# Optimization experiments

Measured on AMD Instinct MI355X. Metric: run time of the kernel, lower is better.

Reference implementation:

```python
import jax, jax.numpy as jnp
import numpy as np

B, T, V, E = 1024, 100, 9173, 100
H1, H2 = 128, 512


def _gru(x, k, rk, b):
    # Keras GRU v2 (reset_after=True). x: [B,T,D], k: [D,3H], rk: [H,3H], b: [2,3H]
    bi, br = b[0], b[1]
    xs = jnp.swapaxes(jnp.einsum('btd,dh->bth', x, k) + bi, 0, 1)  # [T,B,3H]
    H = rk.shape[0]
    h0 = jnp.zeros((x.shape[0], H), x.dtype)

    def step(h, xt):
        inner = h @ rk + br
        xz, xr, xh = jnp.split(xt, 3, -1)
        rz, rr, rh = jnp.split(inner, 3, -1)
        z = jax.nn.sigmoid(xz + rz)
        r = jax.nn.sigmoid(xr + rr)
        hh = jnp.tanh(xh + r * rh)
        h = z * h + (1.0 - z) * hh
        return h, h

    _, ys = jax.lax.scan(step, h0, xs)
    return jnp.swapaxes(ys, 0, 1)  # [B,T,H]


def _lstm(x, k, rk, b, reverse=False):
    # Keras LSTM, gate order i,f,c,o. x: [B,T,D], k: [D,4H], rk: [H,4H], b: [4H]
    if reverse:
        x = x[:, ::-1]
    xs = jnp.swapaxes(jnp.einsum('btd,dh->bth', x, k) + b, 0, 1)  # [T,B,4H]
    H = rk.shape[0]
    Bb = x.shape[0]
    carry0 = (jnp.zeros((Bb, H), x.dtype), jnp.zeros((Bb, H), x.dtype))

    def step(carry, xt):
        h, c = carry
        g = xt + h @ rk
        i, f, cc, o = jnp.split(g, 4, -1)
        c = jax.nn.sigmoid(f) * c + jax.nn.sigmoid(i) * jnp.tanh(cc)
        h = jax.nn.sigmoid(o) * jnp.tanh(c)
        return (h, c), h

    _, ys = jax.lax.scan(step, carry0, xs)
    ys = jnp.swapaxes(ys, 0, 1)
    if reverse:
        ys = ys[:, ::-1]  # Bidirectional re-reverses backward outputs
    return ys


def setup_inputs() -> dict:
    key = jax.random.key(0)
    ks = jax.random.split(key, 32)
    s = 0.05
    p = {}
    p['text'] = jax.random.randint(ks[0], (B, T), 0, V)
    p['upvote'] = jax.random.normal(ks[1], (B, 1), jnp.float32)
    p['emb'] = s * jax.random.normal(ks[2], (V, E), jnp.float32)
    # forward GRU(128)
    p['gf_k'] = s * jax.random.normal(ks[3], (E, 3 * H1), jnp.float32)
    p['gf_rk'] = s * jax.random.normal(ks[4], (H1, 3 * H1), jnp.float32)
    p['gf_b'] = s * jax.random.normal(ks[5], (2, 3 * H1), jnp.float32)
    # backward LSTM(128)
    p['lb_k'] = s * jax.random.normal(ks[6], (E, 4 * H1), jnp.float32)
    p['lb_rk'] = s * jax.random.normal(ks[7], (H1, 4 * H1), jnp.float32)
    p['lb_b'] = s * jax.random.normal(ks[8], (4 * H1,), jnp.float32)
    # GRU(512) on concat(256)
    p['g2_k'] = s * jax.random.normal(ks[9], (2 * H1, 3 * H2), jnp.float32)
    p['g2_rk'] = s * jax.random.normal(ks[10], (H2, 3 * H2), jnp.float32)
    p['g2_b'] = s * jax.random.normal(ks[11], (2, 3 * H2), jnp.float32)
    # LSTM(512)
    p['l2_k'] = s * jax.random.normal(ks[12], (H2, 4 * H2), jnp.float32)
    p['l2_rk'] = s * jax.random.normal(ks[13], (H2, 4 * H2), jnp.float32)
    p['l2_b'] = s * jax.random.normal(ks[14], (4 * H2,), jnp.float32)
    # dense heads
    p['fc1_w'] = s * jax.random.normal(ks[15], (1, 512), jnp.float32)
    p['fc1_b'] = jnp.zeros((512,), jnp.float32)
    p['d1_w'] = s * jax.random.normal(ks[16], (1024, 64), jnp.float32)
    p['d1_b'] = jnp.zeros((64,), jnp.float32)
    p['d2_w'] = s * jax.random.normal(ks[17], (64, 512), jnp.float32)
    p['d2_b'] = jnp.zeros((512,), jnp.float32)
    p['d3_w'] = s * jax.random.normal(ks[18], (512, 128), jnp.float32)
    p['d3_b'] = jnp.zeros((128,), jnp.float32)
    p['rat_w'] = s * jax.random.normal(ks[19], (128, 5), jnp.float32)
    p['rat_b'] = jnp.zeros((5,), jnp.float32)
    p['rec_w'] = s * jax.random.normal(ks[20], (128, 1), jnp.float32)
    p['rec_b'] = jnp.zeros((1,), jnp.float32)
    return p


def reference(text, upvote, emb, gf_k, gf_rk, gf_b, lb_k, lb_rk, lb_b,
              g2_k, g2_rk, g2_b, l2_k, l2_rk, l2_b,
              fc1_w, fc1_b, d1_w, d1_b, d2_w, d2_b, d3_w, d3_b,
              rat_w, rat_b, rec_w, rec_b):
    x = emb[text]                                   # [B,T,E]
    fwd = _gru(x, gf_k, gf_rk, gf_b)                # [B,T,128]
    bwd = _lstm(x, lb_k, lb_rk, lb_b, reverse=True)  # [B,T,128]
    x1 = jnp.concatenate([fwd, bwd], -1)            # [B,T,256]
    x1 = _gru(x1, g2_k, g2_rk, g2_b)                # [B,T,512]
    x1 = _lstm(x1, l2_k, l2_rk, l2_b)               # [B,T,512]
    x1 = jnp.mean(x1, axis=1)                       # GlobalAveragePooling1D
    x2 = jax.nn.relu(upvote @ fc1_w + fc1_b)        # [B,512]
    h = jnp.concatenate([x1, x2], -1)               # [B,1024]
    h = jax.nn.relu(h @ d1_w + d1_b)
    h = jax.nn.relu(h @ d2_w + d2_b)
    h = jax.nn.relu(h @ d3_w + d3_b)
    rating = jax.nn.softmax(h @ rat_w + rat_b, axis=-1)
    recommend = jax.nn.sigmoid(h @ rec_w + rec_b)
    return rating, recommend
```

## Files before the change

### kernel.cpp

```cpp
#include <hip/hip_runtime.h>

typedef __attribute__((ext_vector_type(8))) short bf16x8;
typedef __attribute__((ext_vector_type(4))) float f32x4;

#define MFMA(a, b, c) __builtin_amdgcn_mfma_f32_16x16x32_bf16((a), (b), (c), 0, 0, 0)

__device__ inline short f2bf(float f) {
  unsigned u = __builtin_bit_cast(unsigned, f);
  u += 0x7fffu + ((u >> 16) & 1u);
  return (short)(u >> 16);
}
__device__ inline float bf2f(short s) {
  unsigned u = ((unsigned)(unsigned short)s) << 16;
  return __builtin_bit_cast(float, u);
}
__device__ inline float sigm(float x) { return 1.f / (1.f + expf(-x)); }

#define VM_DRAIN() asm volatile("s_waitcnt vmcnt(0)" ::: "memory")

__device__ __forceinline__ void sc_load16(const char* g0, const char* g1,
                                          const char* l0, const char* l1,
                                          bf16x8* rg, bf16x8* rl) {
  asm volatile(
      "global_load_dwordx4 %0, %16, off sc0 sc1\n\t"
      "global_load_dwordx4 %1, %16, off offset:1024 sc0 sc1\n\t"
      "global_load_dwordx4 %2, %16, off offset:2048 sc0 sc1\n\t"
      "global_load_dwordx4 %3, %16, off offset:3072 sc0 sc1\n\t"
      "global_load_dwordx4 %4, %17, off sc0 sc1\n\t"
      "global_load_dwordx4 %5, %17, off offset:1024 sc0 sc1\n\t"
      "global_load_dwordx4 %6, %17, off offset:2048 sc0 sc1\n\t"
      "global_load_dwordx4 %7, %17, off offset:3072 sc0 sc1\n\t"
      "global_load_dwordx4 %8, %18, off sc0 sc1\n\t"
      "global_load_dwordx4 %9, %18, off offset:1024 sc0 sc1\n\t"
      "global_load_dwordx4 %10, %18, off offset:2048 sc0 sc1\n\t"
      "global_load_dwordx4 %11, %18, off offset:3072 sc0 sc1\n\t"
      "global_load_dwordx4 %12, %19, off sc0 sc1\n\t"
      "global_load_dwordx4 %13, %19, off offset:1024 sc0 sc1\n\t"
      "global_load_dwordx4 %14, %19, off offset:2048 sc0 sc1\n\t"
      "global_load_dwordx4 %15, %19, off offset:3072 sc0 sc1\n\t"
      "s_waitcnt vmcnt(0)"
      : "=&v"(rg[0]), "=&v"(rg[1]), "=&v"(rg[2]), "=&v"(rg[3]),
        "=&v"(rg[4]), "=&v"(rg[5]), "=&v"(rg[6]), "=&v"(rg[7]),
        "=&v"(rl[0]), "=&v"(rl[1]), "=&v"(rl[2]), "=&v"(rl[3]),
        "=&v"(rl[4]), "=&v"(rl[5]), "=&v"(rl[6]), "=&v"(rl[7])
      : "v"(g0), "v"(g1), "v"(l0), "v"(l1)
      : "memory");
}

__device__ __forceinline__ void store_short_sys(short* p, short v) {
  int vi = (int)(unsigned short)v;
  asm volatile("global_store_short %0, %1, off sc0 sc1" :: "v"(p), "v"(vi) : "memory");
}

#define B_SZ 1024
#define T_SZ 100

#define O_GFK   0u
#define O_GFRK  (O_GFK  + 98304u)
#define O_LBK   (O_GFRK + 98304u)
#define O_LBRK  (O_LBK  + 131072u)
#define O_G2    (O_LBRK + 131072u)
#define O_L2    (O_G2   + 2359296u)
#define O_X     (O_L2   + 4194304u)
#define O_X1    (O_X    + 26214400u)
#define O_HG    (O_X1   + 52428800u)
#define O_HL    (O_HG   + 2097152u)
#define O_BAR   (O_HL   + 2097152u)
#define O_MS    (O_BAR  + 2097152u)

__global__ void pack_b(const float* __restrict__ s1, int K1,
                       const float* __restrict__ s2, int K1p,
                       int Kp, int N, short* __restrict__ dst) {
  int i = blockIdx.x * 256 + threadIdx.x;
  int total = N * Kp;
  if (i >= total) return;
  int v = i & 7, c = (i >> 3) & 15, r = i >> 7;
  int kb8 = Kp >> 3;
  int kb = r % kb8, nt = r / kb8;
  int k = kb * 8 + v, col = nt * 16 + c;
  float val;
  if (k < K1p) val = (k < K1) ? s1[k * N + col] : 0.f;
  else         val = s2[(k - K1p) * N + col];
  dst[i] = f2bf(val);
}

__global__ void embed_k(const int* __restrict__ text, const float* __restrict__ emb,
                        short* __restrict__ x) {
  int i = blockIdx.x * 256 + threadIdx.x;
  if (i >= B_SZ * T_SZ * 128) return;
  int col = i & 127, bt = i >> 7;
  float v = 0.f;
  if (col < 100) v = emb[text[bt] * 100 + col];
  x[i] = f2bf(v);
}

__global__ __launch_bounds__(512) void layer1_k(
    const short* __restrict__ x, const short* __restrict__ gfk,
    const short* __restrict__ gfrk, const float* __restrict__ gfb,
    const short* __restrict__ lbk, const short* __restrict__ lbrk,
    const float* __restrict__ lbb, short* __restrict__ x1) {
  __shared__ __attribute__((aligned(16))) short rkl[65536];
  __shared__ __attribute__((aligned(16))) short xst[16 * 136];
  __shared__ __attribute__((aligned(16))) short hst[16 * 136];
  const int wgid = blockIdx.x;
  const bool gru = wgid < 64;
  const int b0 = (gru ? wgid : wgid - 64) * 16;
  const int tid = threadIdx.x, lane = tid & 63, w = tid >> 6;
  const int c = lane & 15, g = lane >> 4;
  const int NS = gru ? 3 : 4;

  for (int i = tid; i < 16 * 136; i += 512) hst[i] = 0;

  const bf16x8* kp = (const bf16x8*)(gru ? gfk : lbk);
  const bf16x8* rpg = (const bf16x8*)(gru ? gfrk : lbrk);
  {
    bf16x8* rl8 = (bf16x8*)rkl;
    int n8 = gru ? 6144 : 8192;
    for (int i = tid; i < n8; i += 512) rl8[i] = rpg[i];
  }
  const bf16x8* rp = (const bf16x8*)rkl;

  bf16x8 kf[4][4];
  #pragma unroll
  for (int s = 0; s < 4; ++s)
    if (s < NS)
      #pragma unroll
      for (int ks = 0; ks < 4; ++ks)
        kf[s][ks] = kp[((s * 8 + w) * 16 + 4 * ks + g) * 16 + c];

  const int col = w * 16 + c;
  float bz = 0, br_ = 0, bxh = 0, brh = 0, bi_ = 0, bf_ = 0, bc_ = 0, bo_ = 0;
  if (gru) {
    bz  = gfb[col]       + gfb[384 + col];
    br_ = gfb[128 + col] + gfb[512 + col];
    bxh = gfb[256 + col];
    brh = gfb[640 + col];
  } else {
    bi_ = lbb[col]; bf_ = lbb[128 + col]; bc_ = lbb[256 + col]; bo_ = lbb[384 + col];
  }

  float hreg[4] = {0.f, 0.f, 0.f, 0.f};
  float cst[4]  = {0.f, 0.f, 0.f, 0.f};

  for (int tt = 0; tt < T_SZ; ++tt) {
    const int t = gru ? tt : (T_SZ - 1 - tt);
    __syncthreads();
    if (tid < 256) {
      int row = tid >> 4, ch = tid & 15;
      *(bf16x8*)&xst[row * 136 + ch * 8] =
          *(const bf16x8*)&x[((b0 + row) * T_SZ + t) * 128 + ch * 8];
    }
    __syncthreads();

    f32x4 acc[4];
    #pragma unroll
    for (int s = 0; s < 4; ++s) acc[s] = (f32x4){0.f, 0.f, 0.f, 0.f};

    bf16x8 ax[4], ah[4];
    #pragma unroll
    for (int ks = 0; ks < 4; ++ks) {
      ax[ks] = *(const bf16x8*)&xst[c * 136 + ks * 32 + g * 8];
      ah[ks] = *(const bf16x8*)&hst[c * 136 + ks * 32 + g * 8];
    }
    #pragma unroll
    for (int s = 0; s < 4; ++s) {
      if (s < NS) {
        int dst = (gru && s == 2) ? 3 : s;
        #pragma unroll
        for (int ks = 0; ks < 4; ++ks) {
          acc[s] = MFMA(ax[ks], kf[s][ks], acc[s]);
          bf16x8 bh = rp[((s * 8 + w) * 16 + 4 * ks + g) * 16 + c];
          acc[dst] = MFMA(ah[ks], bh, acc[dst]);
        }
      }
    }
    __syncthreads();

    if (gru) {
      #pragma unroll
      for (int j = 0; j < 4; ++j) {
        float z  = sigm(acc[0][j] + bz);
        float r  = sigm(acc[1][j] + br_);
        float hh = tanhf(acc[2][j] + bxh + r * (acc[3][j] + brh));
        float hn = z * hreg[j] + (1.f - z) * hh;
        hreg[j] = hn;
        short hb = f2bf(hn);
        int row = 4 * g + j;
        hst[row * 136 + col] = hb;
        x1[((b0 + row) * T_SZ + t) * 256 + col] = hb;
      }
    } else {
      #pragma unroll
      for (int j = 0; j < 4; ++j) {
        float i_ = acc[0][j] + bi_;
        float f_ = acc[1][j] + bf_;
        float cc = acc[2][j] + bc_;
        float o_ = acc[3][j] + bo_;
        float cn = sigm(f_) * cst[j] + sigm(i_) * tanhf(cc);
        cst[j] = cn;
        float hn = sigm(o_) * tanhf(cn);
        short hb = f2bf(hn);
        int row = 4 * g + j;
        hst[row * 136 + col] = hb;
        x1[((b0 + row) * T_SZ + t) * 256 + 128 + col] = hb;
      }
    }
  }
}

__device__ __forceinline__ void gbar16(unsigned* bar, int grp, int gen) {
  VM_DRAIN();
  __syncthreads();
  if (threadIdx.x == 0) {
    unsigned want = (unsigned)(gen + 1);
    unsigned* cnt = bar + grp * 32;
    unsigned* rel = cnt + 16;
    unsigned o = __hip_atomic_fetch_add(cnt, 1u, __ATOMIC_RELAXED, __HIP_MEMORY_SCOPE_AGENT);
    if (o == want * 16u - 1u) {
      __hip_atomic_store(rel, want, __ATOMIC_RELAXED, __HIP_MEMORY_SCOPE_AGENT);
    } else {
      unsigned tries = 0;
      while (__hip_atomic_load(rel, __ATOMIC_RELAXED, __HIP_MEMORY_SCOPE_AGENT) < want) {
        __builtin_amdgcn_s_sleep(2);
        if (++tries > (1u << 22)) break;
      }
    }
  }
  __syncthreads();
}

__global__ __launch_bounds__(512, 2) void persist2_k(
    const short* __restrict__ x1, const short* __restrict__ G2p, const float* __restrict__ g2b,
    const short* __restrict__ L2p, const float* __restrict__ l2b,
    short* __restrict__ hg, short* __restrict__ hl,
    float* __restrict__ msum, unsigned* __restrict__ bar) {
  __shared__ __attribute__((aligned(16))) short Asm[65536];
  float* XA  = (float*)Asm;
  float* XB  = (float*)&Asm[32768];

  const int wgid = blockIdx.x;
  const int rowwg = wgid >> 4, colwg = wgid & 15;
  const int b0 = rowwg * 64;
  const int tid = threadIdx.x, w = tid >> 6, lane = tid & 63;
  const int c = lane & 15, g = lane >> 4;
  const int c7 = c & 7;
  const int ehc = lane & 31;
  const int er0 = w * 8 + (lane >> 5) * 4;
  const int hcg = colwg * 32 + ehc;

  const float bz  = g2b[hcg] + g2b[1536 + hcg];
  const float br_ = g2b[512 + hcg] + g2b[2048 + hcg];
  const float bxh = g2b[1024 + hcg];
  const float brh = g2b[2560 + hcg];
  const float bi_ = l2b[hcg], bf_ = l2b[512 + hcg];
  const float bc_ = l2b[1024 + hcg], bo_ = l2b[1536 + hcg];

  const bf16x8* Gv  = (const bf16x8*)G2p;
  const bf16x8* L2v = (const bf16x8*)L2p;
  const int gw = w >> 1, ghf = w & 1;
  const int gntg = gw * 32 + colwg * 2 + ghf;
  const int lgate = w & 3, lkh = w >> 2;

  float creg[4] = {0.f, 0.f, 0.f, 0.f};
  float mreg[4] = {0.f, 0.f, 0.f, 0.f};

  for (int k = 0; k <= 100; ++k) {
    const short* hg_rd = hg + (size_t)((k + 1) & 1) * 524288;
    const short* hl_rd = hl + (size_t)(k & 1) * 524288;

    if (k < 100) {
      const bf16x8* x1v = (const bf16x8*)x1;
      #pragma unroll
      for (int it = 0; it < 4; ++it) {
        int idx = it * 512 + tid;
        int row = idx >> 5, cx = idx & 31;
        *(bf16x8*)&Asm[32768 + row * 256 + ((cx ^ (row & 7)) << 3)] =
            x1v[((size_t)(b0 + row) * T_SZ + k) * 32 + cx];
      }
    }

    bf16x8 rg[8], rl[8];
    {
      const char* bg = (const char*)hg_rd + (size_t)(b0 + w * 8) * 1024 + lane * 16;
      const char* bl = (const char*)hl_rd + (size_t)(b0 + w * 8) * 1024 + lane * 16;
      sc_load16(bg, bg + 4096, bl, bl + 4096, rg, rl);
    }
    #pragma unroll
    for (int q = 0; q < 8; ++q)
      *(bf16x8*)&Asm[(w * 8 + q) * 512 + ((lane ^ q) << 3)] = rg[q];
    __syncthreads();

    if (k < 100) {
      f32x4 acc[4], acch[4];
      if (w < 6) {
        #pragma unroll
        for (int m = 0; m < 4; ++m) {
          acc[m] = (f32x4){0.f, 0.f, 0.f, 0.f};
          acch[m] = (f32x4){0.f, 0.f, 0.f, 0.f};
        }
        #pragma unroll 6
        for (int ks = 0; ks < 24; ++ks) {
          bf16x8 b = Gv[((size_t)gntg * 96 + 4 * ks + g) * 16 + c];
          bf16x8 a[4];
          #pragma unroll
          for (int m = 0; m < 4; ++m) {
            int row = m * 16 + c;
            a[m] = (ks < 8)
                ? *(const bf16x8*)&Asm[32768 + row * 256 + (((ks * 4 + g) ^ c7) << 3)]
                : *(const bf16x8*)&Asm[row * 512 + ((((ks - 8) * 4 + g) ^ c7) << 3)];
          }
          if (w >= 4 && ks >= 8) {
            #pragma unroll
            for (int m = 0; m < 4; ++m) acch[m] = MFMA(a[m], b, acch[m]);
          } else {
            #pragma unroll
            for (int m = 0; m < 4; ++m) acc[m] = MFMA(a[m], b, acc[m]);
          }
        }
      }
      __syncthreads();

      if (w < 6) {
        #pragma unroll
        for (int m = 0; m < 4; ++m)
          #pragma unroll
          for (int j = 0; j < 4; ++j) {
            int row = m * 16 + 4 * g + j;
            if (gw < 2) XB[(gw * 64 + row) * 36 + ghf * 16 + c] = acc[m][j];
            else {
              XB[(128 + row) * 36 + ghf * 16 + c] = acc[m][j];
              XB[(192 + row) * 36 + ghf * 16 + c] = acch[m][j];
            }
          }
      }
      __syncthreads();

      short* hgw = hg + (size_t)(k & 1) * 524288;
      #pragma unroll
      for (int j = 0; j < 4; ++j) {
        int r = er0 + j;
        int xi = r * 36 + ehc;
        float z  = sigm(XB[xi] + bz);
        float rr = sigm(XB[xi + 2304] + br_);
        float hh = tanhf(XB[xi + 4608] + bxh + rr * (XB[xi + 6912] + brh));
        float hold = bf2f(Asm[r * 512 + (((hcg >> 3) ^ (r & 7)) << 3) + (hcg & 7)]);
        float hn = z * hold + (1.f - z) * hh;
        store_short_sys(&hgw[(size_t)(b0 + r) * 512 + hcg], f2bf(hn));
      }
      __syncthreads();
    }

    if (k >= 1) {
      #pragma unroll
      for (int q = 0; q < 8; ++q)
        *(bf16x8*)&Asm[32768 + (w * 8 + q) * 512 + ((lane ^ q) << 3)] = rl[q];
      __syncthreads();

      f32x4 acc[4][2];
      #pragma unroll
      for (int m = 0; m < 4; ++m)
        #pragma unroll
        for (int n = 0; n < 2; ++n) acc[m][n] = (f32x4){0.f, 0.f, 0.f, 0.f};

      const int abase = lkh ? 32768 : 0;
      #pragma unroll
      for (int ks = 0; ks < 16; ++ks) {
        bf16x8 a[4];
        #pragma unroll
        for (int m = 0; m < 4; ++m) {
          int row = m * 16 + c;
          a[m] = *(const bf16x8*)&Asm[abase + row * 512 + (((ks * 4 + g) ^ c7) << 3)];
        }
        #pragma unroll
        for (int m = 0; m < 4; ++m)
          #pragma unroll
          for (int n = 0; n < 2; ++n) {
            bf16x8 b = L2v[((size_t)(lgate * 32 + colwg * 2 + n) * 128 +
                            4 * (lkh * 16 + ks) + g) * 16 + c];
            acc[m][n] = MFMA(a[m], b, acc[m][n]);
          }
      }
      __syncthreads();

      float* Xp = lkh ? XB : XA;
      #pragma unroll
      for (int m = 0; m < 4; ++m)
        #pragma unroll
        for (int n = 0; n < 2; ++n)
          #pragma unroll
          for (int j = 0; j < 4; ++j)
            Xp[(lgate * 64 + m * 16 + 4 * g + j) * 36 + n * 16 + c] = acc[m][n][j];
      __syncthreads();

      short* hlw = hl + (size_t)((k + 1) & 1) * 524288;
      #pragma unroll
      for (int j = 0; j < 4; ++j) {
        int r = er0 + j;
        int xi = r * 36 + ehc;
        float i_ = XA[xi]        + XB[xi]        + bi_;
        float f_ = XA[xi + 2304] + XB[xi + 2304] + bf_;
        float cc = XA[xi + 4608] + XB[xi + 4608] + bc_;
        float o_ = XA[xi + 6912] + XB[xi + 6912] + bo_;
        float cn = sigm(f_) * creg[j] + sigm(i_) * tanhf(cc);
        creg[j] = cn;
        float hn = sigm(o_) * tanhf(cn);
        mreg[j] += hn;
        store_short_sys(&hlw[(size_t)(b0 + r) * 512 + hcg], f2bf(hn));
      }
    }

    gbar16(bar, rowwg, k);
  }

  #pragma unroll
  for (int j = 0; j < 4; ++j)
    msum[(size_t)(b0 + er0 + j) * 512 + hcg] = mreg[j];
}

__global__ __launch_bounds__(256) void head_k(
    const float* __restrict__ msum, const float* __restrict__ upv,
    const float* __restrict__ fc1w, const float* __restrict__ fc1b,
    const float* __restrict__ d1w, const float* __restrict__ d1b,
    const float* __restrict__ d2w, const float* __restrict__ d2b,
    const float* __restrict__ d3w, const float* __restrict__ d3b,
    const float* __restrict__ rw, const float* __restrict__ rb,
    const float* __restrict__ cw, const float* __restrict__ cb,
    float* __restrict__ out) {
  __shared__ float h[1024], o1[64], o2[512], o3[128], lg[8];
  const int b = blockIdx.x, tid = threadIdx.x;
  const float u = upv[b];
  for (int i = tid; i < 512; i += 256) {
    h[i] = msum[b * 512 + i] * 0.01f;
    float v = u * fc1w[i] + fc1b[i];
    h[512 + i] = v > 0.f ? v : 0.f;
  }
  __syncthreads();
  if (tid < 64) {
    float a = d1b[tid];
    for (int i = 0; i < 1024; ++i) a += h[i] * d1w[i * 64 + tid];
    o1[tid] = a > 0.f ? a : 0.f;
  }
  __syncthreads();
  for (int j = tid; j < 512; j += 256) {
    float a = d2b[j];
    for (int i = 0; i < 64; ++i) a += o1[i] * d2w[i * 512 + j];
    o2[j] = a > 0.f ? a : 0.f;
  }
  __syncthreads();
  if (tid < 128) {
    float a = d3b[tid];
    for (int i = 0; i < 512; ++i) a += o2[i] * d3w[i * 128 + tid];
    o3[tid] = a > 0.f ? a : 0.f;
  }
  __syncthreads();
  if (tid < 5) {
    float a = rb[tid];
    for (int i = 0; i < 128; ++i) a += o3[i] * rw[i * 5 + tid];
    lg[tid] = a;
  }
  if (tid == 5) {
    float a = cb[0];
    for (int i = 0; i < 128; ++i) a += o3[i] * cw[i];
    out[5120 + b] = 1.f / (1.f + expf(-a));
  }
  __syncthreads();
  if (tid == 0) {
    float m = lg[0];
    for (int j = 1; j < 5; ++j) m = fmaxf(m, lg[j]);
    float e[5], s = 0.f;
    for (int j = 0; j < 5; ++j) { e[j] = expf(lg[j] - m); s += e[j]; }
    for (int j = 0; j < 5; ++j) out[b * 5 + j] = e[j] / s;
  }
}

extern "C" void kernel_launch(void* const* d_in, const int* in_sizes, int n_in,
                              void* d_out, int out_size, void* d_ws, size_t ws_size,
                              hipStream_t stream) {
  const int*   text  = (const int*)  d_in[0];
  const float* upv   = (const float*)d_in[1];
  const float* emb   = (const float*)d_in[2];
  const float* gf_k  = (const float*)d_in[3];
  const float* gf_rk = (const float*)d_in[4];
  const float* gf_b  = (const float*)d_in[5];
  const float* lb_k  = (const float*)d_in[6];
  const float* lb_rk = (const float*)d_in[7];
  const float* lb_b  = (const float*)d_in[8];
  const float* g2_k  = (const float*)d_in[9];
  const float* g2_rk = (const float*)d_in[10];
  const float* g2_b  = (const float*)d_in[11];
  const float* l2_k  = (const float*)d_in[12];
  const float* l2_rk = (const float*)d_in[13];
  const float* l2_b  = (const float*)d_in[14];
  const float* fc1_w = (const float*)d_in[15];
  const float* fc1_b = (const float*)d_in[16];
  const float* d1_w  = (const float*)d_in[17];
  const float* d1_b  = (const float*)d_in[18];
  const float* d2_w  = (const float*)d_in[19];
  const float* d2_b  = (const float*)d_in[20];
  const float* d3_w  = (const float*)d_in[21];
  const float* d3_b  = (const float*)d_in[22];
  const float* rat_w = (const float*)d_in[23];
  const float* rat_b = (const float*)d_in[24];
  const float* rec_w = (const float*)d_in[25];
  const float* rec_b = (const float*)d_in[26];

  char* ws = (char*)d_ws;
  short* gfkp  = (short*)(ws + O_GFK);
  short* gfrkp = (short*)(ws + O_GFRK);
  short* lbkp  = (short*)(ws + O_LBK);
  short* lbrkp = (short*)(ws + O_LBRK);
  short* G2p   = (short*)(ws + O_G2);
  short* L2p   = (short*)(ws + O_L2);
  short* xb    = (short*)(ws + O_X);
  short* x1    = (short*)(ws + O_X1);
  short* hg    = (short*)(ws + O_HG);
  short* hl    = (short*)(ws + O_HL);
  unsigned* bar = (unsigned*)(ws + O_BAR);
  float* msum  = (float*)(ws + O_MS);

  pack_b<<<192, 256, 0, stream>>>(gf_k, 100, gf_k, 128, 128, 384, gfkp);
  pack_b<<<192, 256, 0, stream>>>(gf_rk, 128, gf_rk, 128, 128, 384, gfrkp);
  pack_b<<<256, 256, 0, stream>>>(lb_k, 100, lb_k, 128, 128, 512, lbkp);
  pack_b<<<256, 256, 0, stream>>>(lb_rk, 128, lb_rk, 128, 128, 512, lbrkp);
  pack_b<<<4608, 256, 0, stream>>>(g2_k, 256, g2_rk, 256, 768, 1536, G2p);
  pack_b<<<8192, 256, 0, stream>>>(l2_k, 512, l2_rk, 512, 1024, 2048, L2p);

  embed_k<<<51200, 256, 0, stream>>>(text, emb, xb);

  hipMemsetAsync(ws + O_HG + 1048576u, 0, 1048576u, stream);
  hipMemsetAsync(ws + O_HL + 1048576u, 0, 1048576u, stream);
  hipMemsetAsync(ws + O_BAR, 0, 4096u, stream);

  layer1_k<<<128, 512, 0, stream>>>(xb, gfkp, gfrkp, gf_b, lbkp, lbrkp, lb_b, x1);

  {
    const short* x1c = x1; const short* G2c = G2p; const short* L2c = L2p;
    void* kargs[] = {(void*)&x1c, (void*)&G2c, (void*)&g2_b, (void*)&L2c, (void*)&l2_b,
                     (void*)&hg, (void*)&hl, (void*)&msum, (void*)&bar};
    hipError_t e = hipLaunchCooperativeKernel((void*)persist2_k, dim3(256), dim3(512),
                                              kargs, 0, stream);
    if (e != hipSuccess) {
      (void)hipGetLastError();
      persist2_k<<<256, 512, 0, stream>>>(x1c, G2c, g2_b, L2c, l2_b, hg, hl, msum, bar);
    }
  }

  head_k<<<1024, 256, 0, stream>>>(msum, upv, fc1_w, fc1_b, d1_w, d1_b, d2_w, d2_b,
                                   d3_w, d3_b, rat_w, rat_b, rec_w, rec_b,
                                   (float*)d_out);
}
```

Before: 3.235 ms.

## Use per-timestep hidden-state history buffers with plain cached loads

Adds a mode where GRU and LSTM hidden states are written to a separate buffer for each timestep instead of ping-pong double buffers. Because no address is reused across steps, reads can use ordinary cached vector loads instead of sc0/sc1 system-coherent loads, which avoids stale-cache hazards without bypassing caches. It also remaps workgroup IDs so that row groups are interleaved across the grid. The cost is about 200MB of extra workspace, and the mode is enabled only when the workspace is large enough.

```diff
diff --git a/kernel.cpp b/kernel.cpp
--- a/kernel.cpp
+++ b/kernel.cpp
@@ -67,6 +67,9 @@
 #define O_HL    (O_HG   + 2097152u)
 #define O_BAR   (O_HL   + 2097152u)
 #define O_MS    (O_BAR  + 2097152u)
+#define O_HGH   (O_MS   + 2097152u)
+#define O_HLH   (O_HGH  + 105906176u)
+#define WS_NEED (O_HLH + 105906176u)
 
 __global__ void pack_b(const float* __restrict__ s1, int K1,
                        const float* __restrict__ s2, int K1p,
@@ -233,13 +236,14 @@
     const short* __restrict__ x1, const short* __restrict__ G2p, const float* __restrict__ g2b,
     const short* __restrict__ L2p, const float* __restrict__ l2b,
     short* __restrict__ hg, short* __restrict__ hl,
-    float* __restrict__ msum, unsigned* __restrict__ bar) {
+    short* __restrict__ hgH, short* __restrict__ hlH,
+    float* __restrict__ msum, unsigned* __restrict__ bar, int mode) {
   __shared__ __attribute__((aligned(16))) short Asm[65536];
   float* XA  = (float*)Asm;
   float* XB  = (float*)&Asm[32768];
 
   const int wgid = blockIdx.x;
-  const int rowwg = wgid >> 4, colwg = wgid & 15;
+  const int rowwg = wgid & 15, colwg = wgid >> 4;
   const int b0 = rowwg * 64;
   const int tid = threadIdx.x, w = tid >> 6, lane = tid & 63;
   const int c = lane & 15, g = lane >> 4;
@@ -265,8 +269,10 @@
   float mreg[4] = {0.f, 0.f, 0.f, 0.f};
 
   for (int k = 0; k <= 100; ++k) {
-    const short* hg_rd = hg + (size_t)((k + 1) & 1) * 524288;
-    const short* hl_rd = hl + (size_t)(k & 1) * 524288;
+    const short* hg_rd = mode ? hgH + (size_t)k * 524288
+                              : hg + (size_t)((k + 1) & 1) * 524288;
+    const short* hl_rd = mode ? hlH + (size_t)(k >= 1 ? k - 1 : 0) * 524288
+                              : hl + (size_t)(k & 1) * 524288;
 
     if (k < 100) {
       const bf16x8* x1v = (const bf16x8*)x1;
@@ -281,9 +287,16 @@
 
     bf16x8 rg[8], rl[8];
     {
-      const char* bg = (const char*)hg_rd + (size_t)(b0 + w * 8) * 1024 + lane * 16;
-      const char* bl = (const char*)hl_rd + (size_t)(b0 + w * 8) * 1024 + lane * 16;
-      sc_load16(bg, bg + 4096, bl, bl + 4096, rg, rl);
+      const char* bg = (const char*)hg_rd + (size_t)(b0 + w * 8) * 1024 + (size_t)lane * 16;
+      const char* bl = (const char*)hl_rd + (size_t)(b0 + w * 8) * 1024 + (size_t)lane * 16;
+      if (mode) {
+        #pragma unroll
+        for (int q = 0; q < 8; ++q) rg[q] = *(const bf16x8*)(bg + q * 1024);
+        #pragma unroll
+        for (int q = 0; q < 8; ++q) rl[q] = *(const bf16x8*)(bl + q * 1024);
+      } else {
+        sc_load16(bg, bg + 4096, bl, bl + 4096, rg, rl);
+      }
     }
     #pragma unroll
     for (int q = 0; q < 8; ++q)
@@ -335,7 +348,8 @@
       }
       __syncthreads();
 
-      short* hgw = hg + (size_t)(k & 1) * 524288;
+      short* hgw = mode ? hgH + (size_t)(k + 1) * 524288
+                        : hg + (size_t)(k & 1) * 524288;
       #pragma unroll
       for (int j = 0; j < 4; ++j) {
         int r = er0 + j;
@@ -392,7 +406,8 @@
             Xp[(lgate * 64 + m * 16 + 4 * g + j) * 36 + n * 16 + c] = acc[m][n][j];
       __syncthreads();
 
-      short* hlw = hl + (size_t)((k + 1) & 1) * 524288;
+      short* hlw = mode ? hlH + (size_t)k * 524288
+                        : hl + (size_t)((k + 1) & 1) * 524288;
       #pragma unroll
       for (int j = 0; j < 4; ++j) {
         int r = er0 + j;
@@ -517,6 +532,10 @@
   short* hl    = (short*)(ws + O_HL);
   unsigned* bar = (unsigned*)(ws + O_BAR);
   float* msum  = (float*)(ws + O_MS);
+  short* hgH   = (short*)(ws + O_HGH);
+  short* hlH   = (short*)(ws + O_HLH);
+
+  const int mode = (ws_size >= (size_t)WS_NEED) ? 1 : 0;
 
   pack_b<<<192, 256, 0, stream>>>(gf_k, 100, gf_k, 128, 128, 384, gfkp);
   pack_b<<<192, 256, 0, stream>>>(gf_rk, 128, gf_rk, 128, 128, 384, gfrkp);
@@ -527,21 +546,29 @@
 
   embed_k<<<51200, 256, 0, stream>>>(text, emb, xb);
 
-  hipMemsetAsync(ws + O_HG + 1048576u, 0, 1048576u, stream);
-  hipMemsetAsync(ws + O_HL + 1048576u, 0, 1048576u, stream);
   hipMemsetAsync(ws + O_BAR, 0, 4096u, stream);
+  if (mode) {
+    hipMemsetAsync(ws + O_HGH, 0, 1048576u, stream);
+    hipMemsetAsync(ws + O_HLH, 0, 1048576u, stream);
+  } else {
+    hipMemsetAsync(ws + O_HG + 1048576u, 0, 1048576u, stream);
+    hipMemsetAsync(ws + O_HL + 1048576u, 0, 1048576u, stream);
+  }
 
   layer1_k<<<128, 512, 0, stream>>>(xb, gfkp, gfrkp, gf_b, lbkp, lbrkp, lb_b, x1);
 
   {
     const short* x1c = x1; const short* G2c = G2p; const short* L2c = L2p;
+    int modec = mode;
     void* kargs[] = {(void*)&x1c, (void*)&G2c, (void*)&g2_b, (void*)&L2c, (void*)&l2_b,
-                     (void*)&hg, (void*)&hl, (void*)&msum, (void*)&bar};
+                     (void*)&hg, (void*)&hl, (void*)&hgH, (void*)&hlH,
+                     (void*)&msum, (void*)&bar, (void*)&modec};
     hipError_t e = hipLaunchCooperativeKernel((void*)persist2_k, dim3(256), dim3(512),
                                               kargs, 0, stream);
     if (e != hipSuccess) {
       (void)hipGetLastError();
-      persist2_k<<<256, 512, 0, stream>>>(x1c, G2c, g2_b, L2c, l2_b, hg, hl, msum, bar);
+      persist2_k<<<256, 512, 0, stream>>>(x1c, G2c, g2_b, L2c, l2_b, hg, hl, hgH, hlH,
+                                          msum, bar, modec);
     }
   }
 
```

After: 2.989 ms. 7.6% less time.
